# Optimization experiments

Measured on AMD Instinct MI355X. Metric: run time of the kernel, lower is better.

## Reference

```python
import jax, jax.numpy as jnp
import numpy as np

MAX_ITERS = 10


def setup_inputs() -> dict:
    key = jax.random.key(0)
    k1, k2, k3, k4, k5 = jax.random.split(key, 5)
    B, D, H = 8192, 2048, 2048
    s = 1.0 / np.sqrt(H)  # torch default init scale (uniform); we use scaled normal
    return {
        "encoded": jax.random.normal(k1, (B, D), dtype=jnp.float32),
        "w_ih": jax.random.normal(k2, (3 * H, D), dtype=jnp.float32) * s,
        "w_hh": jax.random.normal(k3, (3 * H, H), dtype=jnp.float32) * s,
        "b_ih": jax.random.normal(k4, (3 * H,), dtype=jnp.float32) * s,
        "b_hh": jax.random.normal(k5, (3 * H,), dtype=jnp.float32) * s,
    }


def reference(encoded, w_ih, w_hh, b_ih, b_hh):
    """Iterative GRUCell recurrence (training-mode: full max_iters, no early exit).

    PyTorch GRUCell math:
      r = sigmoid(W_ir x + b_ir + W_hr h + b_hr)
      z = sigmoid(W_iz x + b_iz + W_hz h + b_hz)
      n = tanh(W_in x + b_in + r * (W_hn h + b_hn))
      h' = (1 - z) * n + z * h
    """
    H = w_hh.shape[1]
    # Input projection is constant across iterations (gru_input never changes).
    gi = encoded @ w_ih.T + b_ih  # [B, 3H]
    gi_r, gi_z, gi_n = gi[:, :H], gi[:, H:2 * H], gi[:, 2 * H:]

    def step(h, _):
        gh = h @ w_hh.T + b_hh  # [B, 3H]
        gh_r, gh_z, gh_n = gh[:, :H], gh[:, H:2 * H], gh[:, 2 * H:]
        r = jax.nn.sigmoid(gi_r + gh_r)
        z = jax.nn.sigmoid(gi_z + gh_z)
        n = jnp.tanh(gi_n + r * gh_n)
        h_next = (1.0 - z) * n + z * h
        return h_next, None

    h0 = jnp.zeros((encoded.shape[0], H), dtype=encoded.dtype)
    h, _ = jax.lax.scan(step, h0, None, length=MAX_ITERS)
    return h
```

## Files before the change

kernel.cpp:

```cpp
#include <hip/hip_runtime.h>

typedef _Float16 f16_t;
typedef _Float16 f16x4 __attribute__((ext_vector_type(4)));
typedef _Float16 f16x8 __attribute__((ext_vector_type(8)));
typedef float floatx4 __attribute__((ext_vector_type(4)));

#define GLDS16(gptr, lptr) __builtin_amdgcn_global_load_lds( \
    (const __attribute__((address_space(1))) void*)(gptr),   \
    (__attribute__((address_space(3))) void*)(lptr), 16, 0, 0)

__device__ __forceinline__ float sigmoidf_fast(float x) {
    return 1.f / (1.f + __expf(-x));
}
__device__ __forceinline__ float tanhf_fast(float x) {
    float e = __expf(2.f * x);
    return 1.f - 2.f / (e + 1.f);
}

#define GATE_STRIDE 16777216L

__global__ __launch_bounds__(256)
void cvt_f32_f16(const float* __restrict__ in, f16_t* __restrict__ out, long n)
{
    long i = ((long)blockIdx.x * 256 + threadIdx.x) * 8;
    if (i >= n) return;
    floatx4 a = *(const floatx4*)(in + i);
    floatx4 b = *(const floatx4*)(in + i + 4);
    f16x8 o;
    o[0] = (f16_t)a[0]; o[1] = (f16_t)a[1]; o[2] = (f16_t)a[2]; o[3] = (f16_t)a[3];
    o[4] = (f16_t)b[0]; o[5] = (f16_t)b[1]; o[6] = (f16_t)b[2]; o[7] = (f16_t)b[3];
    *(f16x8*)(out + i) = o;
}

__global__ __launch_bounds__(256, 2)
void gemm_gi(const f16_t* __restrict__ A,
             const f16_t* __restrict__ W,
             const float* __restrict__ bias,
             f16_t* __restrict__ giF)
{
    const int K = 2048;
    __shared__ __align__(16) f16_t As[128 * 32];
    __shared__ __align__(16) f16_t Ws[128 * 32];
    const int tid  = threadIdx.x;
    const int lane = tid & 63;
    const int wave = tid >> 6;
    const int m0 = blockIdx.x * 128;
    const int n0 = blockIdx.y * 128;
    const int wm = (wave >> 1) * 64;
    const int wn = (wave & 1) * 64;

    floatx4 acc[4][4] = {};

    const int srow = lane >> 2;
    const int skc  = (((lane & 3) ^ ((srow >> 1) & 3))) * 8;

    const int fr = lane & 15;
    const int jq = lane >> 4;
    const int jsw = (jq ^ ((fr >> 1) & 3)) * 8;

    for (int k0 = 0; k0 < K; k0 += 32) {
        #pragma unroll
        for (int j = 0; j < 2; ++j) {
            int c = j * 4 + wave;
            int row = c * 16 + srow;
            GLDS16(A + (size_t)(m0 + row) * K + k0 + skc, As + c * 512);
        }
        #pragma unroll
        for (int j = 0; j < 2; ++j) {
            int c = j * 4 + wave;
            int row = c * 16 + srow;
            GLDS16(W + (size_t)(n0 + row) * K + k0 + skc, Ws + c * 512);
        }
        __syncthreads();

        f16x8 a_frag[4], b_frag[4];
        #pragma unroll
        for (int t = 0; t < 4; ++t)
            a_frag[t] = *(const f16x8*)(As + (wm + t * 16 + fr) * 32 + jsw);
        #pragma unroll
        for (int t = 0; t < 4; ++t)
            b_frag[t] = *(const f16x8*)(Ws + (wn + t * 16 + fr) * 32 + jsw);
        #pragma unroll
        for (int tm = 0; tm < 4; ++tm)
            #pragma unroll
            for (int tn = 0; tn < 4; ++tn)
                acc[tm][tn] = __builtin_amdgcn_mfma_f32_16x16x32_f16(
                    a_frag[tm], b_frag[tn], acc[tm][tn], 0, 0, 0);
        __syncthreads();
    }

    const int g   = n0 >> 11;
    const int tNb = ((n0 & 2047) >> 4) + (wn >> 4);
    #pragma unroll
    for (int tm = 0; tm < 4; ++tm) {
        int tM = (m0 + wm + tm * 16) >> 4;
        #pragma unroll
        for (int tn = 0; tn < 4; ++tn) {
            int tN = tNb + tn;
            int n  = n0 + wn + tn * 16 + fr;
            float b = bias[n];
            f16x4 v;
            #pragma unroll
            for (int r = 0; r < 4; ++r) v[r] = (f16_t)(acc[tm][tn][r] + b);
            *(f16x4*)(giF + ((size_t)(g * 512 + tM) * 128 + tN) * 256 + lane * 4) = v;
        }
    }
}

__global__ __launch_bounds__(256)
void gru_init(const f16_t* __restrict__ giF,
              const float* __restrict__ bhh,
              f16_t* __restrict__ h16)
{
    const int H = 2048;
    __shared__ __align__(16) f16_t hp[128 * 72];
    const int tid  = threadIdx.x;
    const int lane = tid & 63;
    const int wave = tid >> 6;
    const int m0 = blockIdx.x * 128;
    const int n0 = blockIdx.y * 64;
    const int wm = (wave >> 1) * 64;
    const int wn = (wave & 1) * 32;
    const int colL = lane & 15;
    const int rq = (lane >> 4) * 4;

    #pragma unroll
    for (int tm = 0; tm < 4; ++tm) {
        int tM = (m0 + wm + tm * 16) >> 4;
        #pragma unroll
        for (int tn = 0; tn < 2; ++tn) {
            int tN = ((n0 + wn) >> 4) + tn;
            size_t base = ((size_t)tM * 128 + tN) * 256 + lane * 4;
            f16x4 g_r = *(const f16x4*)(giF + base);
            f16x4 g_z = *(const f16x4*)(giF + base + GATE_STRIDE);
            f16x4 g_n = *(const f16x4*)(giF + base + 2 * GATE_STRIDE);
            int n = n0 + wn + tn * 16 + colL;
            float br = bhh[n], bz = bhh[H + n], bn = bhh[2 * H + n];
            #pragma unroll
            for (int r = 0; r < 4; ++r) {
                float rr = sigmoidf_fast((float)g_r[r]);
                float zz = sigmoidf_fast((float)g_z[r]);
                float nn = tanhf_fast((float)g_n[r] + rr * bn);
                rr = sigmoidf_fast((float)g_r[r] + br);
                zz = sigmoidf_fast((float)g_z[r] + bz);
                float h = (1.f - zz) * nn;
                hp[(wm + tm * 16 + rq + r) * 72 + wn + tn * 16 + colL] = (f16_t)h;
            }
        }
    }
    __syncthreads();
    #pragma unroll
    for (int i = 0; i < 4; ++i) {
        int r2 = i * 32 + (tid >> 3);
        int ch = tid & 7;
        f16x8 v = *(const f16x8*)(hp + r2 * 72 + ch * 8);
        *(f16x8*)(h16 + (size_t)(m0 + r2) * H + n0 + ch * 8) = v;
    }
}

__global__ __launch_bounds__(256, 2)
void gru_step(const f16_t* __restrict__ Wh,
              const float* __restrict__ bhh,
              const f16_t* __restrict__ giF,
              const f16_t* __restrict__ hin,
              f16_t* __restrict__ hout,
              float* __restrict__ out32)
{
    const int K = 2048, H = 2048;
    __shared__ __align__(16) f16_t smem[128 * 32 + 3 * 64 * 32];
    f16_t* As  = smem;
    f16_t* Wsm = smem + 128 * 32;
    const int tid  = threadIdx.x;
    const int lane = tid & 63;
    const int wave = tid >> 6;
    const int m0 = blockIdx.x * 128;
    const int n0 = blockIdx.y * 64;
    const int wm = (wave >> 1) * 64;
    const int wn = (wave & 1) * 32;

    floatx4 acc[3][4][2] = {};

    const int srow = lane >> 2;
    const int skc  = (((lane & 3) ^ ((srow >> 1) & 3))) * 8;
    const int fr = lane & 15;
    const int jq = lane >> 4;
    const int jsw = (jq ^ ((fr >> 1) & 3)) * 8;

    for (int k0 = 0; k0 < K; k0 += 32) {
        #pragma unroll
        for (int j = 0; j < 2; ++j) {
            int c = j * 4 + wave;
            int row = c * 16 + srow;
            GLDS16(hin + (size_t)(m0 + row) * K + k0 + skc, As + c * 512);
        }
        #pragma unroll
        for (int j = 0; j < 3; ++j) {
            int c = j * 4 + wave;
            int g = c >> 2;
            int ci = c & 3;
            int row = ci * 16 + srow;
            GLDS16(Wh + (size_t)(g * H + n0 + row) * K + k0 + skc,
                   Wsm + c * 512);
        }
        __syncthreads();

        f16x8 a_frag[4];
        #pragma unroll
        for (int t = 0; t < 4; ++t)
            a_frag[t] = *(const f16x8*)(As + (wm + t * 16 + fr) * 32 + jsw);
        #pragma unroll
        for (int g = 0; g < 3; ++g) {
            #pragma unroll
            for (int tn = 0; tn < 2; ++tn) {
                f16x8 b_frag = *(const f16x8*)(Wsm + g * 2048 +
                                               (wn + tn * 16 + fr) * 32 + jsw);
                #pragma unroll
                for (int tm = 0; tm < 4; ++tm)
                    acc[g][tm][tn] = __builtin_amdgcn_mfma_f32_16x16x32_f16(
                        a_frag[tm], b_frag, acc[g][tm][tn], 0, 0, 0);
            }
        }
        __syncthreads();
    }

    const int rq = (lane >> 4) * 4;
    f16x4 hv[4][2];
    #pragma unroll
    for (int tm = 0; tm < 4; ++tm) {
        int tM = (m0 + wm + tm * 16) >> 4;
        #pragma unroll
        for (int tn = 0; tn < 2; ++tn) {
            int tN = ((n0 + wn) >> 4) + tn;
            size_t base = ((size_t)tM * 128 + tN) * 256 + lane * 4;
            f16x4 g_r = *(const f16x4*)(giF + base);
            f16x4 g_z = *(const f16x4*)(giF + base + GATE_STRIDE);
            f16x4 g_n = *(const f16x4*)(giF + base + 2 * GATE_STRIDE);
            int n = n0 + wn + tn * 16 + fr;
            float br = bhh[n], bz = bhh[H + n], bn = bhh[2 * H + n];
            #pragma unroll
            for (int r = 0; r < 4; ++r) {
                int m = m0 + wm + tm * 16 + rq + r;
                float rr = sigmoidf_fast((float)g_r[r] + acc[0][tm][tn][r] + br);
                float zz = sigmoidf_fast((float)g_z[r] + acc[1][tm][tn][r] + bz);
                float nn = tanhf_fast((float)g_n[r] +
                                      rr * (acc[2][tm][tn][r] + bn));
                float hold = (float)hin[(size_t)m * H + n];
                float hnew = (1.f - zz) * nn + zz * hold;
                hv[tm][tn][r] = (f16_t)hnew;
                if (out32) out32[(size_t)m * H + n] = hnew;
            }
        }
    }

    if (!out32) {
        f16_t* hp = smem;
        #pragma unroll
        for (int tm = 0; tm < 4; ++tm)
            #pragma unroll
            for (int tn = 0; tn < 2; ++tn)
                #pragma unroll
                for (int r = 0; r < 4; ++r)
                    hp[(wm + tm * 16 + rq + r) * 72 + wn + tn * 16 + fr] =
                        hv[tm][tn][r];
        __syncthreads();
        #pragma unroll
        for (int i = 0; i < 4; ++i) {
            int r2 = i * 32 + (tid >> 3);
            int ch = tid & 7;
            f16x8 v = *(const f16x8*)(hp + r2 * 72 + ch * 8);
            *(f16x8*)(hout + (size_t)(m0 + r2) * H + n0 + ch * 8) = v;
        }
    }
}

extern "C" void kernel_launch(void* const* d_in, const int* in_sizes, int n_in,
                              void* d_out, int out_size, void* d_ws, size_t ws_size,
                              hipStream_t stream) {
    const float* x    = (const float*)d_in[0];
    const float* w_ih = (const float*)d_in[1];
    const float* w_hh = (const float*)d_in[2];
    const float* b_ih = (const float*)d_in[3];
    const float* b_hh = (const float*)d_in[4];
    float* out = (float*)d_out;

    char* ws = (char*)d_ws;
    f16_t* xh    = (f16_t*)(ws);
    f16_t* wih_h = (f16_t*)(ws + 33554432);
    f16_t* whh_h = (f16_t*)(ws + 33554432 + 25165824);
    f16_t* gi    = (f16_t*)(ws + 33554432 + 2 * 25165824);
    f16_t* h16a  = (f16_t*)(ws + 33554432 + 2 * 25165824 + 100663296);
    f16_t* h16b  = (f16_t*)(ws + 33554432 + 2 * 25165824 + 100663296 + 33554432);

    cvt_f32_f16<<<dim3(8192), 256, 0, stream>>>(x, xh, 16777216L);
    cvt_f32_f16<<<dim3(6144), 256, 0, stream>>>(w_ih, wih_h, 12582912L);
    cvt_f32_f16<<<dim3(6144), 256, 0, stream>>>(w_hh, whh_h, 12582912L);

    gemm_gi<<<dim3(64, 48), 256, 0, stream>>>(xh, wih_h, b_ih, gi);
    gru_init<<<dim3(64, 32), 256, 0, stream>>>(gi, b_hh, h16a);

    f16_t* hin = h16a; f16_t* hout = h16b;
    for (int it = 2; it <= 10; ++it) {
        float* o32 = (it == 10) ? out : nullptr;
        gru_step<<<dim3(64, 32), 256, 0, stream>>>(whh_h, b_hh, gi,
                                                   hin, hout, o32);
        f16_t* t = hin; hin = hout; hout = t;
    }
}
```

Measured before the change: 2.676 ms.

## Deepen gru_step K-tile to 64, remap blocks per XCD, reuse h from LDS

gru_step now stages 64-wide K slices with an XOR-swizzled 8-slot LDS layout, halving the number of barrier pairs per GEMM. Blocks are launched on a 1D grid and remapped so each XCD covers a contiguous band of N columns, which is meant to improve L2 reuse of W_hh. The old hidden state for the gate update is captured from the A tile in LDS when k0 equals n0, replacing a scattered global read in the epilogue. gru_init also drops redundant sigmoid evaluations, and LDS use per block doubles, which may reduce occupancy.

```diff
diff --git a/kernel.cpp b/kernel.cpp
--- a/kernel.cpp
+++ b/kernel.cpp
@@ -53,7 +53,6 @@
 
     const int srow = lane >> 2;
     const int skc  = (((lane & 3) ^ ((srow >> 1) & 3))) * 8;
-
     const int fr = lane & 15;
     const int jq = lane >> 4;
     const int jsw = (jq ^ ((fr >> 1) & 3)) * 8;
@@ -138,11 +137,9 @@
             float br = bhh[n], bz = bhh[H + n], bn = bhh[2 * H + n];
             #pragma unroll
             for (int r = 0; r < 4; ++r) {
-                float rr = sigmoidf_fast((float)g_r[r]);
-                float zz = sigmoidf_fast((float)g_z[r]);
+                float rr = sigmoidf_fast((float)g_r[r] + br);
+                float zz = sigmoidf_fast((float)g_z[r] + bz);
                 float nn = tanhf_fast((float)g_n[r] + rr * bn);
-                rr = sigmoidf_fast((float)g_r[r] + br);
-                zz = sigmoidf_fast((float)g_z[r] + bz);
                 float h = (1.f - zz) * nn;
                 hp[(wm + tm * 16 + rq + r) * 72 + wn + tn * 16 + colL] = (f16_t)h;
             }
@@ -167,63 +164,94 @@
               float* __restrict__ out32)
 {
     const int K = 2048, H = 2048;
-    __shared__ __align__(16) f16_t smem[128 * 32 + 3 * 64 * 32];
+    __shared__ __align__(16) f16_t smem[128 * 64 + 3 * 64 * 64];
     f16_t* As  = smem;
-    f16_t* Wsm = smem + 128 * 32;
+    f16_t* Wsm = smem + 128 * 64;
     const int tid  = threadIdx.x;
     const int lane = tid & 63;
     const int wave = tid >> 6;
-    const int m0 = blockIdx.x * 128;
-    const int n0 = blockIdx.y * 64;
+
+    const int bid   = blockIdx.x;
+    const int xcd   = bid & 7;
+    const int rblk  = bid >> 3;
+    const int m0 = (rblk >> 2) * 128;
+    const int n0 = (xcd * 4 + (rblk & 3)) * 64;
+
     const int wm = (wave >> 1) * 64;
     const int wn = (wave & 1) * 32;
 
     floatx4 acc[3][4][2] = {};
 
-    const int srow = lane >> 2;
-    const int skc  = (((lane & 3) ^ ((srow >> 1) & 3))) * 8;
+    const int srow8 = lane >> 3;
+    const int sgk   = ((lane & 7) ^ srow8) * 8;
     const int fr = lane & 15;
     const int jq = lane >> 4;
-    const int jsw = (jq ^ ((fr >> 1) & 3)) * 8;
-
-    for (int k0 = 0; k0 < K; k0 += 32) {
-        #pragma unroll
-        for (int j = 0; j < 2; ++j) {
+    const int rq = (lane >> 4) * 4;
+
+    f16x4 hold16[4][2];
+
+    for (int k0 = 0; k0 < K; k0 += 64) {
+        #pragma unroll
+        for (int j = 0; j < 4; ++j) {
             int c = j * 4 + wave;
-            int row = c * 16 + srow;
-            GLDS16(hin + (size_t)(m0 + row) * K + k0 + skc, As + c * 512);
-        }
-        #pragma unroll
-        for (int j = 0; j < 3; ++j) {
+            int row = c * 8 + srow8;
+            GLDS16(hin + (size_t)(m0 + row) * K + k0 + sgk, As + c * 512);
+        }
+        #pragma unroll
+        for (int j = 0; j < 6; ++j) {
             int c = j * 4 + wave;
-            int g = c >> 2;
-            int ci = c & 3;
-            int row = ci * 16 + srow;
-            GLDS16(Wh + (size_t)(g * H + n0 + row) * K + k0 + skc,
+            int g = c >> 3;
+            int cw = c & 7;
+            int row = cw * 8 + srow8;
+            GLDS16(Wh + (size_t)(g * H + n0 + row) * K + k0 + sgk,
                    Wsm + c * 512);
         }
         __syncthreads();
 
-        f16x8 a_frag[4];
-        #pragma unroll
-        for (int t = 0; t < 4; ++t)
-            a_frag[t] = *(const f16x8*)(As + (wm + t * 16 + fr) * 32 + jsw);
-        #pragma unroll
-        for (int g = 0; g < 3; ++g) {
-            #pragma unroll
-            for (int tn = 0; tn < 2; ++tn) {
-                f16x8 b_frag = *(const f16x8*)(Wsm + g * 2048 +
-                                               (wn + tn * 16 + fr) * 32 + jsw);
+        if (k0 == n0) {
+            #pragma unroll
+            for (int tm = 0; tm < 4; ++tm) {
                 #pragma unroll
-                for (int tm = 0; tm < 4; ++tm)
-                    acc[g][tm][tn] = __builtin_amdgcn_mfma_f32_16x16x32_f16(
-                        a_frag[tm], b_frag, acc[g][tm][tn], 0, 0, 0);
-            }
-        }
-        __syncthreads();
-    }
-
-    const int rq = (lane >> 4) * 4;
+                for (int tn = 0; tn < 2; ++tn) {
+                    #pragma unroll
+                    for (int r = 0; r < 4; ++r) {
+                        int row_a = wm + tm * 16 + rq + r;
+                        int kloc  = wn + tn * 16 + fr;
+                        int slot  = (kloc >> 3) ^ (row_a & 7);
+                        hold16[tm][tn][r] =
+                            As[row_a * 64 + slot * 8 + (kloc & 7)];
+                    }
+                }
+            }
+        }
+
+        #pragma unroll
+        for (int ksub = 0; ksub < 2; ++ksub) {
+            f16x8 a_frag[4];
+            #pragma unroll
+            for (int t = 0; t < 4; ++t) {
+                int row = wm + t * 16 + fr;
+                int slot = (ksub * 4 + jq) ^ (row & 7);
+                a_frag[t] = *(const f16x8*)(As + row * 64 + slot * 8);
+            }
+            #pragma unroll
+            for (int g = 0; g < 3; ++g) {
+                #pragma unroll
+                for (int tn = 0; tn < 2; ++tn) {
+                    int row_w = wn + tn * 16 + fr;
+                    int slot = (ksub * 4 + jq) ^ (row_w & 7);
+                    f16x8 b_frag = *(const f16x8*)(Wsm + g * 4096 +
+                                                   row_w * 64 + slot * 8);
+                    #pragma unroll
+                    for (int tm = 0; tm < 4; ++tm)
+                        acc[g][tm][tn] = __builtin_amdgcn_mfma_f32_16x16x32_f16(
+                            a_frag[tm], b_frag, acc[g][tm][tn], 0, 0, 0);
+                }
+            }
+        }
+        __syncthreads();
+    }
+
     f16x4 hv[4][2];
     #pragma unroll
     for (int tm = 0; tm < 4; ++tm) {
@@ -244,7 +272,7 @@
                 float zz = sigmoidf_fast((float)g_z[r] + acc[1][tm][tn][r] + bz);
                 float nn = tanhf_fast((float)g_n[r] +
                                       rr * (acc[2][tm][tn][r] + bn));
-                float hold = (float)hin[(size_t)m * H + n];
+                float hold = (float)hold16[tm][tn][r];
                 float hnew = (1.f - zz) * nn + zz * hold;
                 hv[tm][tn][r] = (f16_t)hnew;
                 if (out32) out32[(size_t)m * H + n] = hnew;
@@ -301,8 +329,8 @@
     f16_t* hin = h16a; f16_t* hout = h16b;
     for (int it = 2; it <= 10; ++it) {
         float* o32 = (it == 10) ? out : nullptr;
-        gru_step<<<dim3(64, 32), 256, 0, stream>>>(whh_h, b_hh, gi,
-                                                   hin, hout, o32);
+        gru_step<<<dim3(2048), 256, 0, stream>>>(whh_h, b_hh, gi,
+                                                 hin, hout, o32);
         f16_t* t = hin; hin = hout; hout = t;
     }
 }
```

Result: faster. 2.525 ms (-5.7%).
